# Kernel tuning notes

Hardware: AMD Instinct MI355X
Metric: run time of the kernel (lower is better)

The kernel has to match this reference:

```python
import jax, jax.numpy as jnp
import numpy as np

D = 256; NH = 8; HD = 32; DFF = 1024; NL = 4; NPT = 4
SHAPES = [(100, 100), (50, 50), (25, 25), (13, 13)]
LEN_V = sum(h * w for h, w in SHAPES)  # 13294
BS = 16; LQ = 300


def _ln(x, g, b):
    m = jnp.mean(x, -1, keepdims=True)
    v = jnp.var(x, -1, keepdims=True)
    return (x - m) * jax.lax.rsqrt(v + 1e-5) * g + b


def _bilinear(v, loc, H, W):
    # v: [bs, nh, H*W, hd]; loc: [bs, Lq, nh, P, 2] normalized [0,1]
    # matches F.grid_sample(bilinear, align_corners=False, padding_mode='zeros')
    bs, Lq, nh, P, _ = loc.shape
    x = loc[..., 0] * W - 0.5
    y = loc[..., 1] * H - 0.5
    x0 = jnp.floor(x); y0 = jnp.floor(y)
    dx = x - x0; dy = y - y0
    x0 = x0.astype(jnp.int32); y0 = y0.astype(jnp.int32)
    out = jnp.zeros((bs, Lq, nh, P, v.shape[-1]), v.dtype)
    for ix, iy, w in ((x0, y0, (1 - dx) * (1 - dy)),
                      (x0 + 1, y0, dx * (1 - dy)),
                      (x0, y0 + 1, (1 - dx) * dy),
                      (x0 + 1, y0 + 1, dx * dy)):
        valid = (ix >= 0) & (ix < W) & (iy >= 0) & (iy < H)
        idx = jnp.clip(iy, 0, H - 1) * W + jnp.clip(ix, 0, W - 1)  # [bs,Lq,nh,P]
        idx = jnp.transpose(idx, (0, 2, 1, 3)).reshape(bs, nh, Lq * P, 1)
        g = jnp.take_along_axis(v, idx, axis=2).reshape(bs, nh, Lq, P, -1)
        g = jnp.transpose(g, (0, 2, 1, 3, 4))  # [bs,Lq,nh,P,hd]
        out = out + g * jnp.where(valid, w, jnp.zeros_like(w))[..., None]
    return out


def reference(tgt, reference_points, memory, Wq, bq, Wk, bk, Wv, bv, Wo, bo,
              Wvp, bvp, Wso, bso, Waw, baw, Wop, bop, W1, bf1, W2, bf2,
              ln1_g, ln1_b, ln2_g, ln2_b, ln3_g, ln3_b):
    bs, Lq, _ = tgt.shape
    # ---- self attention (query_pos_embed=None, attn_mask=None) ----
    qh = (tgt @ Wq + bq).reshape(bs, Lq, NH, HD)
    kh = (tgt @ Wk + bk).reshape(bs, Lq, NH, HD)
    vh = (tgt @ Wv + bv).reshape(bs, Lq, NH, HD)
    scores = jnp.einsum('bqhd,bkhd->bhqk', qh, kh) * np.float32(1.0 / np.sqrt(HD))
    attn = jax.nn.softmax(scores, -1)
    sa = jnp.einsum('bhqk,bkhd->bqhd', attn, vh).reshape(bs, Lq, D) @ Wo + bo
    t = _ln(tgt + sa, ln1_g, ln1_b)
    # ---- PP multi-scale deformable cross attention ----
    val = (memory @ Wvp + bvp).reshape(bs, LEN_V, NH, HD)
    val = jnp.transpose(val, (0, 2, 1, 3))  # [bs, nh, Lv, hd]
    off = (t @ Wso + bso).reshape(bs, Lq, NH, NL, NPT, 2)
    aw = jax.nn.softmax((t @ Waw + baw).reshape(bs, Lq, NH, NL * NPT), -1)
    aw = aw.reshape(bs, Lq, NH, NL, NPT)
    rp = reference_points  # [bs, Lq, NL, 4] -> (cx, cy, w, h) branch
    loc = rp[:, :, None, :, None, :2] + off / NPT * rp[:, :, None, :, None, 2:] * 0.5
    start = 0
    ca = jnp.zeros((bs, Lq, NH, HD), t.dtype)
    for l, (H, W) in enumerate(SHAPES):
        v_l = val[:, :, start:start + H * W]
        sampled = _bilinear(v_l, loc[:, :, :, l], H, W)  # [bs,Lq,nh,P,hd]
        ca = ca + jnp.einsum('bqhpd,bqhp->bqhd', sampled, aw[:, :, :, l])
        start += H * W
    ca = ca.reshape(bs, Lq, D) @ Wop + bop
    t = _ln(t + ca, ln2_g, ln2_b)
    # ---- FFN ----
    ff = jax.nn.relu(t @ W1 + bf1) @ W2 + bf2
    return _ln(t + ff, ln3_g, ln3_b)


def setup_inputs() -> dict:
    ks = iter(jax.random.split(jax.random.key(0), 64))
    inp = {}
    inp['tgt'] = jax.random.normal(next(ks), (BS, LQ, D), jnp.float32)
    inp['reference_points'] = jax.random.uniform(next(ks), (BS, LQ, NL, 4), jnp.float32)
    inp['memory'] = jax.random.normal(next(ks), (BS, LEN_V, D), jnp.float32)
    for name, sh in [('Wq', (D, D)), ('Wk', (D, D)), ('Wv', (D, D)), ('Wo', (D, D)),
                     ('Wvp', (D, D)), ('Wso', (D, NH * NL * NPT * 2)),
                     ('Waw', (D, NH * NL * NPT)), ('Wop', (D, D)),
                     ('W1', (D, DFF)), ('W2', (DFF, D))]:
        inp[name] = jax.random.normal(next(ks), sh, jnp.float32) * 0.02
    for name, dim in [('bq', D), ('bk', D), ('bv', D), ('bo', D), ('bvp', D),
                      ('bso', NH * NL * NPT * 2), ('baw', NH * NL * NPT),
                      ('bop', D), ('bf1', DFF), ('bf2', D)]:
        inp[name] = jnp.zeros((dim,), jnp.float32)
    for g, b in [('ln1_g', 'ln1_b'), ('ln2_g', 'ln2_b'), ('ln3_g', 'ln3_b')]:
        inp[g] = jnp.ones((D,), jnp.float32)
        inp[b] = jnp.zeros((D,), jnp.float32)
    return inp
```

## Files before the change

### kernel.cpp

```cpp
#include <hip/hip_runtime.h>
#include <hip/hip_bf16.h>
#include <cstddef>

#define D_    256
#define NH_   8
#define HD_   32
#define LQ_   300
#define BS_   16
#define LENV_ 13294
#define DFF_  1024
#define NROWS (BS_*LQ_)
#define VROWS (BS_*LENV_)

typedef __attribute__((ext_vector_type(8))) short short8;
typedef __attribute__((ext_vector_type(4))) float f32x4;
typedef unsigned int u32;

__device__ __forceinline__ short f2bf(float x) {
    unsigned u = __float_as_uint(x);
    u += 0x7fff + ((u >> 16) & 1);
    return (short)(u >> 16);
}
__device__ __forceinline__ unsigned pack_bf2(float lo, float hi) {
    return (unsigned)(unsigned short)f2bf(lo) | ((unsigned)(unsigned short)f2bf(hi) << 16);
}

__global__ __launch_bounds__(256) void prep_all(
    const float* __restrict__ Wq, const float* __restrict__ Wk,
    const float* __restrict__ Wv, const float* __restrict__ Wo,
    const float* __restrict__ Wvp, const float* __restrict__ Wso,
    const float* __restrict__ Waw, const float* __restrict__ Wop,
    const float* __restrict__ W1, const float* __restrict__ W2,
    const float* __restrict__ bqp, const float* __restrict__ bkp,
    const float* __restrict__ bvp, const float* __restrict__ bsop,
    const float* __restrict__ bawp,
    short* __restrict__ Wqkvt, short* __restrict__ Wot,
    short* __restrict__ Wvpt, short* __restrict__ Wsoawt,
    short* __restrict__ Wopt, short* __restrict__ W1t,
    short* __restrict__ W2t, float* __restrict__ bqkv,
    float* __restrict__ bsoaw)
{
    const int blk = blockIdx.x, tid = threadIdx.x;
    if (blk < 1792) {
        const int seg = blk >> 8;
        const int e = ((blk & 255) << 8) | tid;
        const int n = e >> 8, k = e & 255;
        const float* src; short* dst;
        switch (seg) {
            case 0: src = Wq;  dst = Wqkvt;          break;
            case 1: src = Wk;  dst = Wqkvt + 65536;  break;
            case 2: src = Wv;  dst = Wqkvt + 131072; break;
            case 3: src = Wo;  dst = Wot;            break;
            case 4: src = Wvp; dst = Wvpt;           break;
            case 5: src = Wso; dst = Wsoawt;         break;
            default: src = Wop; dst = Wopt;          break;
        }
        dst[e] = f2bf(src[(size_t)k * 256 + n]);
    } else if (blk < 1920) {
        const int e = ((blk - 1792) << 8) | tid;
        const int n = e >> 8, k = e & 255;
        Wsoawt[65536 + e] = f2bf(Waw[(size_t)k * 128 + n]);
    } else if (blk < 2048) {
        const int e = ((blk - 1920) << 8) | tid;
        Wsoawt[98304 + e] = 0;
    } else if (blk < 3072) {
        const int e = ((blk - 2048) << 8) | tid;
        const int n = e >> 8, k = e & 255;
        W1t[e] = f2bf(W1[(size_t)k * 1024 + n]);
    } else if (blk < 4096) {
        const int e = ((blk - 3072) << 8) | tid;
        const int n = e / 1024, k = e % 1024;
        W2t[e] = f2bf(W2[(size_t)k * 256 + n]);
    } else {
        const int e = ((blk - 4096) << 8) | tid;
        if (e < 768)
            bqkv[e] = (e < 256) ? bqp[e] : (e < 512) ? bkp[e - 256] : bvp[e - 512];
        else if (e < 1280) {
            const int f = e - 768;
            bsoaw[f] = (f < 256) ? bsop[f] : (f < 384) ? bawp[f - 256] : 0.f;
        }
    }
}

template<int ACT, int OUT_BF16, int STACKED>
__global__ __launch_bounds__(256) void mfma_gemm(
    const float* __restrict__ A, const short* __restrict__ Wt,
    const float* __restrict__ bias, void* __restrict__ Cout,
    int M, int N, int K)
{
    __shared__ short Alds[2][64 * 40];
    __shared__ short Blds[2][256 * 40];
    const int tid  = threadIdx.x;
    const int lane = tid & 63;
    const int wn   = tid >> 6;
    const int m0   = blockIdx.x * 64;
    const int nb   = blockIdx.y;
    const int srow = tid >> 2;
    const int schk = tid & 3;

    const int  arow = m0 + srow;
    const bool aok  = (arow < M);
    const float* aptr = &A[(size_t)(aok ? arow : 0) * K + schk * 8];
    const short* bptr = &Wt[(size_t)(nb * 256 + srow) * K + schk * 8];

    f32x4 acc[4][4] = {};
    float4 ra0, ra1;
    short8 rb0, rb1, rb2, rb3;

    ra0 = make_float4(0.f, 0.f, 0.f, 0.f); ra1 = ra0;
    if (aok) { ra0 = *(const float4*)(aptr); ra1 = *(const float4*)(aptr + 4); }
    rb0 = *(const short8*)(bptr);
    rb1 = *(const short8*)(bptr + (size_t)64 * K);
    rb2 = *(const short8*)(bptr + (size_t)128 * K);
    rb3 = *(const short8*)(bptr + (size_t)192 * K);
    {
        short8 s;
        s[0] = f2bf(ra0.x); s[1] = f2bf(ra0.y); s[2] = f2bf(ra0.z); s[3] = f2bf(ra0.w);
        s[4] = f2bf(ra1.x); s[5] = f2bf(ra1.y); s[6] = f2bf(ra1.z); s[7] = f2bf(ra1.w);
        *(short8*)&Alds[0][srow * 40 + schk * 8] = s;
        *(short8*)&Blds[0][(srow +   0) * 40 + schk * 8] = rb0;
        *(short8*)&Blds[0][(srow +  64) * 40 + schk * 8] = rb1;
        *(short8*)&Blds[0][(srow + 128) * 40 + schk * 8] = rb2;
        *(short8*)&Blds[0][(srow + 192) * 40 + schk * 8] = rb3;
    }
    __syncthreads();

    const int lg = lane >> 4;
    const int lr = lane & 15;
    int buf = 0;

    for (int k0 = 32; k0 < K; k0 += 32) {
        ra0 = make_float4(0.f, 0.f, 0.f, 0.f); ra1 = ra0;
        if (aok) { ra0 = *(const float4*)(aptr + k0); ra1 = *(const float4*)(aptr + k0 + 4); }
        rb0 = *(const short8*)(bptr + k0);
        rb1 = *(const short8*)(bptr + k0 + (size_t)64 * K);
        rb2 = *(const short8*)(bptr + k0 + (size_t)128 * K);
        rb3 = *(const short8*)(bptr + k0 + (size_t)192 * K);

        {
            short8 a[4], b[4];
            #pragma unroll
            for (int mr = 0; mr < 4; ++mr)
                a[mr] = *(const short8*)&Alds[buf][(mr * 16 + lr) * 40 + lg * 8];
            #pragma unroll
            for (int nr = 0; nr < 4; ++nr)
                b[nr] = *(const short8*)&Blds[buf][(wn * 64 + nr * 16 + lr) * 40 + lg * 8];
            #pragma unroll
            for (int mr = 0; mr < 4; ++mr)
                #pragma unroll
                for (int nr = 0; nr < 4; ++nr)
                    acc[mr][nr] = __builtin_amdgcn_mfma_f32_16x16x32_bf16(
                        a[mr], b[nr], acc[mr][nr], 0, 0, 0);
        }

        {
            short8 s;
            s[0] = f2bf(ra0.x); s[1] = f2bf(ra0.y); s[2] = f2bf(ra0.z); s[3] = f2bf(ra0.w);
            s[4] = f2bf(ra1.x); s[5] = f2bf(ra1.y); s[6] = f2bf(ra1.z); s[7] = f2bf(ra1.w);
            const int ob = buf ^ 1;
            *(short8*)&Alds[ob][srow * 40 + schk * 8] = s;
            *(short8*)&Blds[ob][(srow +   0) * 40 + schk * 8] = rb0;
            *(short8*)&Blds[ob][(srow +  64) * 40 + schk * 8] = rb1;
            *(short8*)&Blds[ob][(srow + 128) * 40 + schk * 8] = rb2;
            *(short8*)&Blds[ob][(srow + 192) * 40 + schk * 8] = rb3;
        }
        __syncthreads();
        buf ^= 1;
    }

    {
        short8 a[4], b[4];
        #pragma unroll
        for (int mr = 0; mr < 4; ++mr)
            a[mr] = *(const short8*)&Alds[buf][(mr * 16 + lr) * 40 + lg * 8];
        #pragma unroll
        for (int nr = 0; nr < 4; ++nr)
            b[nr] = *(const short8*)&Blds[buf][(wn * 64 + nr * 16 + lr) * 40 + lg * 8];
        #pragma unroll
        for (int mr = 0; mr < 4; ++mr)
            #pragma unroll
            for (int nr = 0; nr < 4; ++nr)
                acc[mr][nr] = __builtin_amdgcn_mfma_f32_16x16x32_bf16(
                    a[mr], b[nr], acc[mr][nr], 0, 0, 0);
    }

    if (STACKED) {
        float* Cb = (float*)Cout + (size_t)nb * M * 256;
        const float* bb = bias + nb * 256;
        #pragma unroll
        for (int mr = 0; mr < 4; ++mr)
            #pragma unroll
            for (int r = 0; r < 4; ++r) {
                const int row = m0 + mr * 16 + lg * 4 + r;
                if (row >= M) continue;
                #pragma unroll
                for (int nr = 0; nr < 4; ++nr) {
                    const int col = wn * 64 + nr * 16 + lr;
                    Cb[(size_t)row * 256 + col] = acc[mr][nr][r] + bb[col];
                }
            }
    } else {
        #pragma unroll
        for (int mr = 0; mr < 4; ++mr)
            #pragma unroll
            for (int r = 0; r < 4; ++r) {
                const int row = m0 + mr * 16 + lg * 4 + r;
                if (row >= M) continue;
                #pragma unroll
                for (int nr = 0; nr < 4; ++nr) {
                    const int col = nb * 256 + wn * 64 + nr * 16 + lr;
                    float v = acc[mr][nr][r] + bias[col];
                    if (ACT) v = fmaxf(v, 0.f);
                    if (OUT_BF16) ((short*)Cout)[(size_t)row * N + col] = f2bf(v);
                    else          ((float*)Cout)[(size_t)row * N + col] = v;
                }
            }
    }
}

__global__ __launch_bounds__(256, 1) void vp_gemm(
    const float* __restrict__ A, const short* __restrict__ Wt,
    const float* __restrict__ bias, short* __restrict__ C)
{
    __shared__ float Alds[2][64 * 256];
    const int tid  = threadIdx.x;
    const int lane = tid & 63;
    const int w    = tid >> 6;
    const int lr   = lane & 15;
    const int lg   = lane >> 4;

    short8 bf[4][8];
    #pragma unroll
    for (int nr = 0; nr < 4; ++nr) {
        const short* wp = &Wt[(size_t)(w * 64 + nr * 16 + lr) * 256 + lg * 8];
        #pragma unroll
        for (int kc = 0; kc < 8; ++kc)
            bf[nr][kc] = *(const short8*)(wp + kc * 32);
    }
    float bs[4];
    #pragma unroll
    for (int nr = 0; nr < 4; ++nr) bs[nr] = bias[w * 64 + nr * 16 + lr];

    const int NT = (VROWS + 63) / 64;
    int t = blockIdx.x;
    int buf = 0;

    #define VP_STAGE(BUFI, TILE)                                               \
        {                                                                      \
            _Pragma("unroll")                                                  \
            for (int j = 0; j < 16; ++j) {                                     \
                const int r = w * 16 + j;                                      \
                int grow = (TILE) * 64 + r;                                    \
                grow = min(grow, VROWS - 1);                                   \
                const int c16 = ((((lane >> 1) ^ (r & 7)) << 1) | (lane & 1)); \
                const float* src = A + (size_t)grow * 256 + c16 * 4;           \
                __builtin_amdgcn_global_load_lds(                              \
                    (const __attribute__((address_space(1))) u32*)src,         \
                    (__attribute__((address_space(3))) u32*)&Alds[BUFI][r*256],\
                    16, 0, 0);                                                 \
            }                                                                  \
        }

    VP_STAGE(0, t);
    __syncthreads();

    while (true) {
        const int t2 = t + 256;
        if (t2 < NT) VP_STAGE(buf ^ 1, t2);

        f32x4 acc[4][4] = {};
        #pragma unroll
        for (int kc = 0; kc < 8; ++kc) {
            short8 a[4];
            #pragma unroll
            for (int mr = 0; mr < 4; ++mr) {
                const int row = mr * 16 + lr;
                const int c32 = (kc * 4 + lg) ^ (row & 7);
                const float* p = &Alds[buf][row * 256 + c32 * 8];
                float4 x = *(const float4*)(p);
                float4 y = *(const float4*)(p + 4);
                short8 s;
                s[0] = f2bf(x.x); s[1] = f2bf(x.y); s[2] = f2bf(x.z); s[3] = f2bf(x.w);
                s[4] = f2bf(y.x); s[5] = f2bf(y.y); s[6] = f2bf(y.z); s[7] = f2bf(y.w);
                a[mr] = s;
            }
            #pragma unroll
            for (int mr = 0; mr < 4; ++mr)
                #pragma unroll
                for (int nr = 0; nr < 4; ++nr)
                    acc[mr][nr] = __builtin_amdgcn_mfma_f32_16x16x32_bf16(
                        a[mr], bf[nr][kc], acc[mr][nr], 0, 0, 0);
        }

        #pragma unroll
        for (int mr = 0; mr < 4; ++mr)
            #pragma unroll
            for (int r4 = 0; r4 < 4; ++r4) {
                const int row = t * 64 + mr * 16 + lg * 4 + r4;
                if (row >= VROWS) continue;
                #pragma unroll
                for (int nr = 0; nr < 4; ++nr)
                    C[(size_t)row * 256 + w * 64 + nr * 16 + lr] =
                        f2bf(acc[mr][nr][r4] + bs[nr]);
            }

        __syncthreads();
        buf ^= 1;
        if (t2 >= NT) break;
        t = t2;
    }
    #undef VP_STAGE
}

__global__ __launch_bounds__(256) void attn_fused(
    const float* __restrict__ qh, const float* __restrict__ kh,
    const float* __restrict__ vh, float* __restrict__ sa)
{
    __shared__ short Klds[304 * 40];
    __shared__ short Vtlds[32 * 328];
    const int bh = blockIdx.x, b = bh / NH_, h = bh % NH_;
    const int tid = threadIdx.x;

    for (int idx = tid; idx < 304 * 4; idx += 256) {
        const int key = idx >> 2, dc = idx & 3;
        short8 s = {};
        if (key < LQ_) {
            const float* kp = &kh[((size_t)(b * LQ_ + key)) * D_ + h * HD_ + dc * 8];
            float4 a0 = *reinterpret_cast<const float4*>(kp);
            float4 a1 = *reinterpret_cast<const float4*>(kp + 4);
            s[0] = f2bf(a0.x); s[1] = f2bf(a0.y); s[2] = f2bf(a0.z); s[3] = f2bf(a0.w);
            s[4] = f2bf(a1.x); s[5] = f2bf(a1.y); s[6] = f2bf(a1.z); s[7] = f2bf(a1.w);
        }
        *reinterpret_cast<short8*>(&Klds[key * 40 + dc * 8]) = s;
    }
    for (int idx = tid; idx < LQ_ * 8; idx += 256) {
        const int key = idx >> 3, dc = idx & 7;
        const float4 v4 = *reinterpret_cast<const float4*>(
            &vh[((size_t)(b * LQ_ + key)) * D_ + h * HD_ + dc * 4]);
        Vtlds[(dc * 4 + 0) * 328 + key] = f2bf(v4.x);
        Vtlds[(dc * 4 + 1) * 328 + key] = f2bf(v4.y);
        Vtlds[(dc * 4 + 2) * 328 + key] = f2bf(v4.z);
        Vtlds[(dc * 4 + 3) * 328 + key] = f2bf(v4.w);
    }
    for (int idx = tid; idx < 32 * 20; idx += 256) {
        const int d = idx / 20, kk = idx % 20;
        Vtlds[d * 328 + 300 + kk] = 0;
    }
    __syncthreads();

    const int lane = tid & 63;
    const int wid  = tid >> 6;
    const int g    = lane >> 4;
    const int qc   = lane & 15;
    const int y    = blockIdx.y;
    const int qt_end = (y == 0) ? 10 : 19;

    for (int qt = y * 10 + wid; qt < qt_end; qt += 4) {
        const int q0 = qt * 16;
        short8 qf;
        {
            const int q = min(q0 + qc, LQ_ - 1);
            const float* qp = &qh[((size_t)(b * LQ_ + q)) * D_ + h * HD_ + g * 8];
            float4 a0 = *reinterpret_cast<const float4*>(qp);
            float4 a1 = *reinterpret_cast<const float4*>(qp + 4);
            const float sc = 0.17677669529663687f;
            qf[0] = f2bf(a0.x * sc); qf[1] = f2bf(a0.y * sc);
            qf[2] = f2bf(a0.z * sc); qf[3] = f2bf(a0.w * sc);
            qf[4] = f2bf(a1.x * sc); qf[5] = f2bf(a1.y * sc);
            qf[6] = f2bf(a1.z * sc); qf[7] = f2bf(a1.w * sc);
        }
        f32x4 s[19];
        #pragma unroll
        for (int kt = 0; kt < 19; ++kt) {
            short8 kf = *reinterpret_cast<const short8*>(&Klds[(kt * 16 + qc) * 40 + g * 8]);
            f32x4 z = {};
            s[kt] = __builtin_amdgcn_mfma_f32_16x16x32_bf16(kf, qf, z, 0, 0, 0);
        }
        if (g == 3) { s[18][0] = -1e30f; s[18][1] = -1e30f; s[18][2] = -1e30f; s[18][3] = -1e30f; }

        float m = -1e30f;
        #pragma unroll
        for (int kt = 0; kt < 19; ++kt)
            #pragma unroll
            for (int r = 0; r < 4; ++r) m = fmaxf(m, s[kt][r]);
        m = fmaxf(m, __shfl_xor(m, 16));
        m = fmaxf(m, __shfl_xor(m, 32));
        float sum = 0.f;
        #pragma unroll
        for (int kt = 0; kt < 19; ++kt)
            #pragma unroll
            for (int r = 0; r < 4; ++r) {
                float e = __expf(s[kt][r] - m);
                s[kt][r] = e; sum += e;
            }
        sum += __shfl_xor(sum, 16);
        sum += __shfl_xor(sum, 32);
        const float inv = 1.f / sum;

        unsigned pb0[20], pb1[20];
        #pragma unroll
        for (int kt = 0; kt < 19; ++kt) {
            pb0[kt] = pack_bf2(s[kt][0] * inv, s[kt][1] * inv);
            pb1[kt] = pack_bf2(s[kt][2] * inv, s[kt][3] * inv);
        }
        pb0[19] = 0; pb1[19] = 0;

        f32x4 acc0 = {}, acc1 = {};
        const int src0 = ((g & 1) << 5) + qc;
        const int src1 = src0 + 16;
        const bool hi = (g >> 1);
        #pragma unroll
        for (int c = 0; c < 10; ++c) {
            short8 va0 = *reinterpret_cast<const short8*>(&Vtlds[qc * 328 + c * 32 + g * 8]);
            short8 va1 = *reinterpret_cast<const short8*>(&Vtlds[(qc + 16) * 328 + c * 32 + g * 8]);
            int x0a = __shfl((int)pb0[2 * c], src0), x0b = __shfl((int)pb0[2 * c + 1], src0);
            int x1a = __shfl((int)pb1[2 * c], src0), x1b = __shfl((int)pb1[2 * c + 1], src0);
            int x2a = __shfl((int)pb0[2 * c], src1), x2b = __shfl((int)pb0[2 * c + 1], src1);
            int x3a = __shfl((int)pb1[2 * c], src1), x3b = __shfl((int)pb1[2 * c + 1], src1);
            union { int u[4]; short8 s8; } pb;
            pb.u[0] = hi ? x0b : x0a;
            pb.u[1] = hi ? x1b : x1a;
            pb.u[2] = hi ? x2b : x2a;
            pb.u[3] = hi ? x3b : x3a;
            acc0 = __builtin_amdgcn_mfma_f32_16x16x32_bf16(va0, pb.s8, acc0, 0, 0, 0);
            acc1 = __builtin_amdgcn_mfma_f32_16x16x32_bf16(va1, pb.s8, acc1, 0, 0, 0);
        }

        if (q0 + qc < LQ_) {
            float* op = &sa[((size_t)(b * LQ_ + q0 + qc)) * D_ + h * HD_ + 4 * g];
            *reinterpret_cast<float4*>(op)      = make_float4(acc0[0], acc0[1], acc0[2], acc0[3]);
            *reinterpret_cast<float4*>(op + 16) = make_float4(acc1[0], acc1[1], acc1[2], acc1[3]);
        }
    }
}

__global__ __launch_bounds__(64) void ln_kernel(
    const float* __restrict__ x, const float* __restrict__ res,
    const float* __restrict__ g, const float* __restrict__ bb,
    float* __restrict__ out)
{
    const size_t row = blockIdx.x;
    const int lane = threadIdx.x;
    const float* xp = x + row * D_;
    const float* rp = res + row * D_;
    float v[4], s = 0.f, s2 = 0.f;
    #pragma unroll
    for (int j = 0; j < 4; ++j) {
        v[j] = xp[lane + j * 64] + rp[lane + j * 64];
        s += v[j]; s2 += v[j] * v[j];
    }
    #pragma unroll
    for (int o = 32; o; o >>= 1) { s += __shfl_xor(s, o); s2 += __shfl_xor(s2, o); }
    const float mean = s * (1.f / D_);
    const float var  = s2 * (1.f / D_) - mean * mean;
    const float inv  = rsqrtf(var + 1e-5f);
    #pragma unroll
    for (int j = 0; j < 4; ++j) {
        int c = lane + j * 64;
        out[row * D_ + c] = (v[j] - mean) * inv * g[c] + bb[c];
    }
}

__global__ __launch_bounds__(256) void deform_kernel(
    const __hip_bfloat16* __restrict__ val, const float* __restrict__ off,
    const float* __restrict__ aw, const float* __restrict__ rp,
    float* __restrict__ ca)
{
    const int i = blockIdx.x * 256 + threadIdx.x;
    if (i >= NROWS * NH_ * 8) return;
    const int dq = i & 7;
    const int h  = (i >> 3) & 7;
    const int bq = i >> 6;
    const int b  = bq / LQ_;

    const int Hs[4] = {100, 50, 25, 13};
    const int st[4] = {0, 10000, 12500, 13125};

    const float* rpp  = rp  + (size_t)bq * 16;
    const float* offp = off + (size_t)bq * 256 + h * 32;
    const float* awp  = aw  + (size_t)bq * 256 + h * 16;
    const ushort* vb  = (const ushort*)val + ((size_t)b * LENV_) * D_ + h * HD_ + dq * 4;

    float wv[16], wmax = -1e30f, wsum = 0.f;
    #pragma unroll
    for (int j = 0; j < 16; ++j) { wv[j] = awp[j]; wmax = fmaxf(wmax, wv[j]); }
    #pragma unroll
    for (int j = 0; j < 16; ++j) { wv[j] = __expf(wv[j] - wmax); wsum += wv[j]; }
    const float winv = 1.f / wsum;

    float a0 = 0.f, a1 = 0.f, a2 = 0.f, a3 = 0.f;
    #pragma unroll
    for (int l = 0; l < 4; ++l) {
        const float cx = rpp[l * 4 + 0], cy = rpp[l * 4 + 1];
        const float sw = rpp[l * 4 + 2], sh = rpp[l * 4 + 3];
        const int H = Hs[l], W = Hs[l];
        const int base = st[l];
        #pragma unroll
        for (int p = 0; p < 4; ++p) {
            const float ox = offp[l * 8 + p * 2 + 0];
            const float oy = offp[l * 8 + p * 2 + 1];
            const float x = (cx + ox * 0.125f * sw) * W - 0.5f;
            const float y = (cy + oy * 0.125f * sh) * H - 0.5f;
            const float x0f = floorf(x), y0f = floorf(y);
            const float dx = x - x0f, dy = y - y0f;
            const int x0 = (int)x0f, y0 = (int)y0f;
            const float a = wv[l * 4 + p] * winv;

            float t0 = 0.f, t1 = 0.f, t2 = 0.f, t3 = 0.f;
            #pragma unroll
            for (int t = 0; t < 4; ++t) {
                const int ix = x0 + (t & 1);
                const int iy = y0 + (t >> 1);
                const float wx = (t & 1) ? dx : (1.f - dx);
                const float wy = (t >> 1) ? dy : (1.f - dy);
                const bool valid = (ix >= 0) & (ix < W) & (iy >= 0) & (iy < H);
                const int cxi = min(max(ix, 0), W - 1);
                const int cyi = min(max(iy, 0), H - 1);
                const float w = valid ? wx * wy : 0.f;
                const ushort4 u = *reinterpret_cast<const ushort4*>(
                    &vb[(size_t)(base + cyi * W + cxi) * D_]);
                t0 = fmaf(w, __uint_as_float((unsigned)u.x << 16), t0);
                t1 = fmaf(w, __uint_as_float((unsigned)u.y << 16), t1);
                t2 = fmaf(w, __uint_as_float((unsigned)u.z << 16), t2);
                t3 = fmaf(w, __uint_as_float((unsigned)u.w << 16), t3);
            }
            a0 = fmaf(a, t0, a0); a1 = fmaf(a, t1, a1);
            a2 = fmaf(a, t2, a2); a3 = fmaf(a, t3, a3);
        }
    }
    *reinterpret_cast<float4*>(&ca[(size_t)i * 4]) = make_float4(a0, a1, a2, a3);
}

extern "C" void kernel_launch(void* const* d_in, const int* in_sizes, int n_in,
                              void* d_out, int out_size, void* d_ws, size_t ws_size,
                              hipStream_t stream)
{
    const float* tgt    = (const float*)d_in[0];
    const float* refpts = (const float*)d_in[1];
    const float* memory = (const float*)d_in[2];
    const float* Wq  = (const float*)d_in[3];
    const float* Wk  = (const float*)d_in[4];
    const float* Wv  = (const float*)d_in[5];
    const float* Wo  = (const float*)d_in[6];
    const float* Wvp = (const float*)d_in[7];
    const float* Wso = (const float*)d_in[8];
    const float* Waw = (const float*)d_in[9];
    const float* Wop = (const float*)d_in[10];
    const float* W1  = (const float*)d_in[11];
    const float* W2  = (const float*)d_in[12];
    const float* bq  = (const float*)d_in[13];
    const float* bk  = (const float*)d_in[14];
    const float* bv  = (const float*)d_in[15];
    const float* bo  = (const float*)d_in[16];
    const float* bvp = (const float*)d_in[17];
    const float* bso = (const float*)d_in[18];
    const float* baw = (const float*)d_in[19];
    const float* bop = (const float*)d_in[20];
    const float* bf1 = (const float*)d_in[21];
    const float* bf2 = (const float*)d_in[22];
    const float* ln1g = (const float*)d_in[23];
    const float* ln1b = (const float*)d_in[24];
    const float* ln2g = (const float*)d_in[25];
    const float* ln2b = (const float*)d_in[26];
    const float* ln3g = (const float*)d_in[27];
    const float* ln3b = (const float*)d_in[28];
    float* out = (float*)d_out;

    const size_t SZ = (size_t)NROWS * D_;
    float* ws = (float*)d_ws;
    float* reg1 = ws;
    float* reg2 = ws + SZ;
    float* reg3 = ws + 2 * SZ;
    float* t    = ws + 3 * SZ;
    float* t2   = ws + 4 * SZ;
    float* big  = ws + 5 * SZ;

    float* qh = reg1;
    float* kh = reg2;
    float* vh = reg3;
    float* sa_heads = t2;
    float* sa_o = big;
    __hip_bfloat16* val = (__hip_bfloat16*)big;
    float* off_raw = reg2;
    float* aw_raw  = reg3;
    float* ca_heads = reg1;
    float* ca_o = reg2;
    float* ff1 = big;
    float* ff2 = reg1;

    char* wtbase = (char*)d_ws + 5 * SZ * sizeof(float) + (size_t)VROWS * D_ * 2;
    short* Wqkvt  = (short*)wtbase;
    short* Wot    = Wqkvt  + 196608;
    short* Wvpt   = Wot    + 65536;
    short* Wsoawt = Wvpt   + 65536;
    short* Wopt   = Wsoawt + 131072;
    short* W1t    = Wopt   + 65536;
    short* W2t    = W1t    + 262144;
    float* bqkv   = (float*)(W2t + 262144);
    float* bsoaw  = bqkv + 768;

    const dim3 blk(256);

    prep_all<<<dim3(4101), blk, 0, stream>>>(
        Wq, Wk, Wv, Wo, Wvp, Wso, Waw, Wop, W1, W2,
        bq, bk, bv, bso, baw,
        Wqkvt, Wot, Wvpt, Wsoawt, Wopt, W1t, W2t, bqkv, bsoaw);

    mfma_gemm<0,0,1><<<dim3(75, 3), blk, 0, stream>>>(tgt, Wqkvt, bqkv, reg1, NROWS, 256, D_);

    attn_fused<<<dim3(BS_ * NH_, 2), blk, 0, stream>>>(qh, kh, vh, sa_heads);

    mfma_gemm<0,0,0><<<dim3(75, 1), blk, 0, stream>>>(sa_heads, Wot, bo, sa_o, NROWS, 256, D_);
    ln_kernel<<<dim3(NROWS), dim3(64), 0, stream>>>(sa_o, tgt, ln1g, ln1b, t);

    vp_gemm<<<dim3(256), blk, 0, stream>>>(memory, Wvpt, bvp, (short*)val);

    mfma_gemm<0,0,1><<<dim3(75, 2), blk, 0, stream>>>(t, Wsoawt, bsoaw, reg2, NROWS, 256, D_);

    deform_kernel<<<dim3((NROWS * NH_ * 8 + 255) / 256), blk, 0, stream>>>(
        val, off_raw, aw_raw, refpts, ca_heads);

    mfma_gemm<0,0,0><<<dim3(75, 1), blk, 0, stream>>>(ca_heads, Wopt, bop, ca_o, NROWS, 256, D_);
    ln_kernel<<<dim3(NROWS), dim3(64), 0, stream>>>(ca_o, t, ln2g, ln2b, t2);

    mfma_gemm<1,0,0><<<dim3(75, 4), blk, 0, stream>>>(t2, W1t, bf1, ff1, NROWS, DFF_, D_);
    mfma_gemm<0,0,0><<<dim3(75, 1), blk, 0, stream>>>(ff1, W2t, bf2, ff2, NROWS, 256, DFF_);
    ln_kernel<<<dim3(NROWS), dim3(64), 0, stream>>>(ff2, t2, ln3g, ln3b, out);
}
```

Baseline: 244.1 us.

## Halve vp_gemm tile for two blocks per CU, stage output via LDS; widen deform loads

```diff
diff --git a/kernel.cpp b/kernel.cpp
--- a/kernel.cpp
+++ b/kernel.cpp
@@ -23,6 +23,9 @@
 }
 __device__ __forceinline__ unsigned pack_bf2(float lo, float hi) {
     return (unsigned)(unsigned short)f2bf(lo) | ((unsigned)(unsigned short)f2bf(hi) << 16);
+}
+__device__ __forceinline__ float bf2f(short s) {
+    return __uint_as_float((unsigned)(unsigned short)s << 16);
 }
 
 __global__ __launch_bounds__(256) void prep_all(
@@ -218,11 +221,12 @@
     }
 }
 
-__global__ __launch_bounds__(256, 1) void vp_gemm(
+__global__ __launch_bounds__(256, 2) void vp_gemm(
     const float* __restrict__ A, const short* __restrict__ Wt,
     const float* __restrict__ bias, short* __restrict__ C)
 {
-    __shared__ float Alds[2][64 * 256];
+    __shared__ float Alds[2][32 * 256];
+    __shared__ short Cst[32 * 256];
     const int tid  = threadIdx.x;
     const int lane = tid & 63;
     const int w    = tid >> 6;
@@ -241,17 +245,17 @@
     #pragma unroll
     for (int nr = 0; nr < 4; ++nr) bs[nr] = bias[w * 64 + nr * 16 + lr];
 
-    const int NT = (VROWS + 63) / 64;
+    const int NT = VROWS / 32;
+    const int NB = 512;
     int t = blockIdx.x;
     int buf = 0;
 
     #define VP_STAGE(BUFI, TILE)                                               \
         {                                                                      \
             _Pragma("unroll")                                                  \
-            for (int j = 0; j < 16; ++j) {                                     \
-                const int r = w * 16 + j;                                      \
-                int grow = (TILE) * 64 + r;                                    \
-                grow = min(grow, VROWS - 1);                                   \
+            for (int j = 0; j < 8; ++j) {                                      \
+                const int r = w * 8 + j;                                       \
+                const int grow = (TILE) * 32 + r;                              \
                 const int c16 = ((((lane >> 1) ^ (r & 7)) << 1) | (lane & 1)); \
                 const float* src = A + (size_t)grow * 256 + c16 * 4;           \
                 __builtin_amdgcn_global_load_lds(                              \
@@ -265,15 +269,15 @@
     __syncthreads();
 
     while (true) {
-        const int t2 = t + 256;
+        const int t2 = t + NB;
         if (t2 < NT) VP_STAGE(buf ^ 1, t2);
 
-        f32x4 acc[4][4] = {};
+        f32x4 acc[2][4] = {};
         #pragma unroll
         for (int kc = 0; kc < 8; ++kc) {
-            short8 a[4];
-            #pragma unroll
-            for (int mr = 0; mr < 4; ++mr) {
+            short8 a[2];
+            #pragma unroll
+            for (int mr = 0; mr < 2; ++mr) {
                 const int row = mr * 16 + lr;
                 const int c32 = (kc * 4 + lg) ^ (row & 7);
                 const float* p = &Alds[buf][row * 256 + c32 * 8];
@@ -285,7 +289,7 @@
                 a[mr] = s;
             }
             #pragma unroll
-            for (int mr = 0; mr < 4; ++mr)
+            for (int mr = 0; mr < 2; ++mr)
                 #pragma unroll
                 for (int nr = 0; nr < 4; ++nr)
                     acc[mr][nr] = __builtin_amdgcn_mfma_f32_16x16x32_bf16(
@@ -293,17 +297,24 @@
         }
 
         #pragma unroll
-        for (int mr = 0; mr < 4; ++mr)
-            #pragma unroll
-            for (int r4 = 0; r4 < 4; ++r4) {
-                const int row = t * 64 + mr * 16 + lg * 4 + r4;
-                if (row >= VROWS) continue;
+        for (int mr = 0; mr < 2; ++mr)
+            #pragma unroll
+            for (int r4 = 0; r4 < 4; ++r4)
                 #pragma unroll
                 for (int nr = 0; nr < 4; ++nr)
-                    C[(size_t)row * 256 + w * 64 + nr * 16 + lr] =
+                    Cst[(mr * 16 + lg * 4 + r4) * 256 + w * 64 + nr * 16 + lr] =
                         f2bf(acc[mr][nr][r4] + bs[nr]);
+        __syncthreads();
+
+        {
+            const size_t base = (size_t)t * 32 * 256;
+            #pragma unroll
+            for (int j = 0; j < 4; ++j) {
+                const int chunk = j * 256 + tid;
+                *(short8*)&C[base + (size_t)chunk * 8] =
+                    *(const short8*)&Cst[chunk * 8];
             }
-
+        }
         __syncthreads();
         buf ^= 1;
         if (t2 >= NT) break;
@@ -467,10 +478,10 @@
     float* __restrict__ ca)
 {
     const int i = blockIdx.x * 256 + threadIdx.x;
-    if (i >= NROWS * NH_ * 8) return;
-    const int dq = i & 7;
-    const int h  = (i >> 3) & 7;
-    const int bq = i >> 6;
+    if (i >= NROWS * NH_ * 4) return;
+    const int dq = i & 3;
+    const int h  = (i >> 2) & 7;
+    const int bq = i >> 5;
     const int b  = bq / LQ_;
 
     const int Hs[4] = {100, 50, 25, 13};
@@ -479,7 +490,7 @@
     const float* rpp  = rp  + (size_t)bq * 16;
     const float* offp = off + (size_t)bq * 256 + h * 32;
     const float* awp  = aw  + (size_t)bq * 256 + h * 16;
-    const ushort* vb  = (const ushort*)val + ((size_t)b * LENV_) * D_ + h * HD_ + dq * 4;
+    const short* vb   = (const short*)val + ((size_t)b * LENV_) * D_ + h * HD_ + dq * 8;
 
     float wv[16], wmax = -1e30f, wsum = 0.f;
     #pragma unroll
@@ -488,7 +499,7 @@
     for (int j = 0; j < 16; ++j) { wv[j] = __expf(wv[j] - wmax); wsum += wv[j]; }
     const float winv = 1.f / wsum;
 
-    float a0 = 0.f, a1 = 0.f, a2 = 0.f, a3 = 0.f;
+    float acc[8] = {};
     #pragma unroll
     for (int l = 0; l < 4; ++l) {
         const float cx = rpp[l * 4 + 0], cy = rpp[l * 4 + 1];
@@ -506,7 +517,7 @@
             const int x0 = (int)x0f, y0 = (int)y0f;
             const float a = wv[l * 4 + p] * winv;
 
-            float t0 = 0.f, t1 = 0.f, t2 = 0.f, t3 = 0.f;
+            float tp[8] = {};
             #pragma unroll
             for (int t = 0; t < 4; ++t) {
                 const int ix = x0 + (t & 1);
@@ -517,18 +528,20 @@
                 const int cxi = min(max(ix, 0), W - 1);
                 const int cyi = min(max(iy, 0), H - 1);
                 const float w = valid ? wx * wy : 0.f;
-                const ushort4 u = *reinterpret_cast<const ushort4*>(
+                const short8 u = *reinterpret_cast<const short8*>(
                     &vb[(size_t)(base + cyi * W + cxi) * D_]);
-                t0 = fmaf(w, __uint_as_float((unsigned)u.x << 16), t0);
-                t1 = fmaf(w, __uint_as_float((unsigned)u.y << 16), t1);
-                t2 = fmaf(w, __uint_as_float((unsigned)u.z << 16), t2);
-                t3 = fmaf(w, __uint_as_float((unsigned)u.w << 16), t3);
+                #pragma unroll
+                for (int k = 0; k < 8; ++k)
+                    tp[k] = fmaf(w, bf2f(u[k]), tp[k]);
             }
-            a0 = fmaf(a, t0, a0); a1 = fmaf(a, t1, a1);
-            a2 = fmaf(a, t2, a2); a3 = fmaf(a, t3, a3);
-        }
-    }
-    *reinterpret_cast<float4*>(&ca[(size_t)i * 4]) = make_float4(a0, a1, a2, a3);
+            #pragma unroll
+            for (int k = 0; k < 8; ++k)
+                acc[k] = fmaf(a, tp[k], acc[k]);
+        }
+    }
+    float* op = &ca[(size_t)i * 8];
+    *reinterpret_cast<float4*>(op)     = make_float4(acc[0], acc[1], acc[2], acc[3]);
+    *reinterpret_cast<float4*>(op + 4) = make_float4(acc[4], acc[5], acc[6], acc[7]);
 }
 
 extern "C" void kernel_launch(void* const* d_in, const int* in_sizes, int n_in,
@@ -613,11 +626,11 @@
     mfma_gemm<0,0,0><<<dim3(75, 1), blk, 0, stream>>>(sa_heads, Wot, bo, sa_o, NROWS, 256, D_);
     ln_kernel<<<dim3(NROWS), dim3(64), 0, stream>>>(sa_o, tgt, ln1g, ln1b, t);
 
-    vp_gemm<<<dim3(256), blk, 0, stream>>>(memory, Wvpt, bvp, (short*)val);
+    vp_gemm<<<dim3(512), blk, 0, stream>>>(memory, Wvpt, bvp, (short*)val);
 
     mfma_gemm<0,0,1><<<dim3(75, 2), blk, 0, stream>>>(t, Wsoawt, bsoaw, reg2, NROWS, 256, D_);
 
-    deform_kernel<<<dim3((NROWS * NH_ * 8 + 255) / 256), blk, 0, stream>>>(
+    deform_kernel<<<dim3((NROWS * NH_ * 4 + 255) / 256), blk, 0, stream>>>(
         val, off_raw, aw_raw, refpts, ca_heads);
 
     mfma_gemm<0,0,0><<<dim3(75, 1), blk, 0, stream>>>(ca_heads, Wopt, bop, ca_o, NROWS, 256, D_);
```

After: 226.6 us. -7.2%, faster.
